# Performance work log

Measured on AMD Instinct MI355X. Metric: run time of the kernel, lower is better.

Reference implementation:

```python
import jax, jax.numpy as jnp
import numpy as np

NEG_SLOPE = 0.01  # torch F.leaky_relu default


def _mlp_block(x, mask, W, b):
    # x: [B,P,V,F]; mask: [B,P,V] bool; W: [H,F]; b: [H]
    h = jax.nn.leaky_relu(jnp.einsum('bpvf,hf->bpvh', x, W) + b, NEG_SLOPE)
    m = mask[..., None]
    out = jnp.where(m, h, 0.0)                                   # zeros at masked-out slots
    neg = jnp.where(m, out, -jnp.inf)
    pool = jnp.max(neg, axis=2, keepdims=True)                   # [B,P,1,H] masked max-pool
    any_valid = jnp.any(mask, axis=2)[:, :, None, None]
    pool = jnp.where(any_valid, pool, 0.0)                       # fully-masked polylines -> 0
    rep = jnp.broadcast_to(pool, out.shape)
    return jnp.concatenate([out, rep], axis=-1)                  # [B,P,V,2H]


def setup_inputs() -> dict:
    key = jax.random.key(0)
    ks = jax.random.split(key, 8)
    B, P, V, F, H = 32, 512, 32, 16, 64
    input_var = jax.random.normal(ks[0], (B, P, V, F), dtype=jnp.float32)
    input_mask = jax.random.bernoulli(ks[1], 0.8, (B, P, V))
    s = 1.0 / np.sqrt(F)
    W1 = jax.random.uniform(ks[2], (H, F), jnp.float32, -s, s)
    b1 = jax.random.uniform(ks[3], (H,), jnp.float32, -s, s)
    s2 = 1.0 / np.sqrt(2 * H)
    W2 = jax.random.uniform(ks[4], (H, 2 * H), jnp.float32, -s2, s2)
    b2 = jax.random.uniform(ks[5], (H,), jnp.float32, -s2, s2)
    W3 = jax.random.uniform(ks[6], (H, 2 * H), jnp.float32, -s2, s2)
    b3 = jax.random.uniform(ks[7], (H,), jnp.float32, -s2, s2)
    return {"input_var": input_var, "input_mask": input_mask,
            "W1": W1, "b1": b1, "W2": W2, "b2": b2, "W3": W3, "b3": b3,
            "size1": P, "size2": V}


def reference(input_var, input_mask, W1, b1, W2, b2, W3, b3, size1, size2):
    hidden = W1.shape[0]
    x = _mlp_block(input_var, input_mask, W1, b1)
    y = _mlp_block(x, input_mask, W2, b2)
    z = _mlp_block(y, input_mask, W3, b3)
    out = z[:, :, 0, -hidden:]                                   # pooled half, same across V
    out = jnp.where(jnp.any(input_mask, axis=2)[..., None], out, 0.0)
    return out
```

## Files before the change

kernel.cpp:

```cpp
#include <hip/hip_runtime.h>
#include <math.h>

namespace {
constexpr int kXS = 72;
constexpr float kSlope = 0.01f;

typedef short bf16x8 __attribute__((ext_vector_type(8)));
typedef float f32x4  __attribute__((ext_vector_type(4)));

__device__ __forceinline__ float lrelu(float x) { return fmaxf(x, kSlope * x); }

__device__ __forceinline__ unsigned short bfrne(float a) {
    union { float f; unsigned u; } v; v.f = a;
    return (unsigned short)((v.u + 0x7FFFu + ((v.u >> 16) & 1u)) >> 16);
}

__global__ void prep_weights(const float* __restrict__ W1,
                             const float* __restrict__ W2,
                             const float* __restrict__ W3,
                             unsigned short* __restrict__ ws)
{
    int t = blockIdx.x * blockDim.x + threadIdx.x;
    if (t >= 36 * 64) return;
    int f = t >> 6, l = t & 63, c = l & 15, q = l >> 4;
    unsigned short v[8] = {0, 0, 0, 0, 0, 0, 0, 0};
    const float* src = nullptr; int row = 0, k0 = 0, K = 0;
    if (f < 4) {
        if (q < 2) { src = W1; row = 16 * f + c; k0 = q * 8; K = 16; }
    } else if (f < 20) {
        int g = f - 4;  src = W2; row = 16 * (g >> 2) + c; k0 = (g & 3) * 32 + q * 8; K = 128;
    } else {
        int g = f - 20; src = W3; row = 16 * (g >> 2) + c; k0 = (g & 3) * 32 + q * 8; K = 128;
    }
    if (src) {
        #pragma unroll
        for (int j = 0; j < 8; ++j) v[j] = bfrne(src[row * K + k0 + j]);
    }
    unsigned short* dst = ws + (size_t)f * 512 + l * 8;
    *(ushort4*)(dst)     = make_ushort4(v[0], v[1], v[2], v[3]);
    *(ushort4*)(dst + 4) = make_ushort4(v[4], v[5], v[6], v[7]);
}

__global__ __launch_bounds__(256, 4) void fused_mlp_v5(
    const float* __restrict__ X, const int* __restrict__ M,
    const unsigned short* __restrict__ WF,
    const float* __restrict__ B1, const float* __restrict__ B2,
    const float* __restrict__ B3, float* __restrict__ OUT)
{
    __shared__ __align__(16) short sX[4][2][32 * kXS];
    __shared__ __align__(16) short sP[4][2][64];

    const int t = threadIdx.x, w = t >> 6, l = t & 63, c = l & 15, q = l >> 4;
    const size_t bp = (size_t)blockIdx.x * 4 + w;

    short* xb2 = &sX[w][0][0]; short* pl2 = &sP[w][0][0];
    short* xb3 = &sX[w][1][0]; short* pl3 = &sP[w][1][0];

    float4 xr[2][2];
    if (q < 2) {
        #pragma unroll
        for (int mt = 0; mt < 2; ++mt) {
            const float4* p = (const float4*)(X + (bp * 32 + 16 * mt + c) * 16 + q * 8);
            xr[mt][0] = p[0]; xr[mt][1] = p[1];
        }
    }
    const int4* Mp = (const int4*)(M + bp * 32);
    const int4 mr0 = Mp[q], mr1 = Mp[4 + q];
    const unsigned mbits =
        (mr0.x ? 1u : 0u)  | (mr0.y ? 2u : 0u)  | (mr0.z ? 4u : 0u)  | (mr0.w ? 8u : 0u) |
        (mr1.x ? 16u : 0u) | (mr1.y ? 32u : 0u) | (mr1.z ? 64u : 0u) | (mr1.w ? 128u : 0u);
    const bool anyv = __any(mbits != 0);

    float bias1[4], bias2[4], bias3[4];
    #pragma unroll
    for (int nt = 0; nt < 4; ++nt) {
        bias1[nt] = B1[16 * nt + c];
        bias2[nt] = B2[16 * nt + c];
        bias3[nt] = B3[16 * nt + c];
    }

    f32x4 acc[2][4];

    {
        bf16x8 a1f[2];
        #pragma unroll
        for (int mt = 0; mt < 2; ++mt) {
            bf16x8 v = {};
            if (q < 2) {
                float4 f0 = xr[mt][0], f1 = xr[mt][1];
                v[0] = (short)bfrne(f0.x); v[1] = (short)bfrne(f0.y);
                v[2] = (short)bfrne(f0.z); v[3] = (short)bfrne(f0.w);
                v[4] = (short)bfrne(f1.x); v[5] = (short)bfrne(f1.y);
                v[6] = (short)bfrne(f1.z); v[7] = (short)bfrne(f1.w);
            }
            a1f[mt] = v;
        }
        #pragma unroll
        for (int nt = 0; nt < 4; ++nt) {
            bf16x8 wf = *(const bf16x8*)(WF + (size_t)nt * 512 + l * 8);
            f32x4 c0 = { bias1[nt], bias1[nt], bias1[nt], bias1[nt] };
            acc[0][nt] = __builtin_amdgcn_mfma_f32_16x16x32_bf16(a1f[0], wf, c0, 0, 0, 0);
            acc[1][nt] = __builtin_amdgcn_mfma_f32_16x16x32_bf16(a1f[1], wf, c0, 0, 0, 0);
        }
    }

    auto epilogue = [&](short* xb, short* pl) {
        float pool[4];
        #pragma unroll
        for (int nt = 0; nt < 4; ++nt) {
            float pv = -INFINITY;
            #pragma unroll
            for (int mt = 0; mt < 2; ++mt) {
                short* base = &xb[(16 * mt + 4 * q) * kXS + 16 * nt + c];
                #pragma unroll
                for (int r = 0; r < 4; ++r) {
                    float y = lrelu(acc[mt][nt][r]);
                    bool mk = (mbits >> (mt * 4 + r)) & 1;
                    float o = mk ? y : 0.f;
                    pv = mk ? fmaxf(pv, y) : pv;
                    base[r * kXS] = (short)bfrne(o);
                }
            }
            pv = fmaxf(pv, __shfl_xor(pv, 16));
            pv = fmaxf(pv, __shfl_xor(pv, 32));
            pool[nt] = anyv ? pv : 0.f;
        }
        float ps = (q & 2) ? ((q & 1) ? pool[3] : pool[2])
                           : ((q & 1) ? pool[1] : pool[0]);
        pl[16 * q + c] = (short)bfrne(ps);
    };

    auto layerK = [&](const short* xb, const short* pl, int fb, const float (&bias)[4]) {
        bf16x8 a00 = *(const bf16x8*)&xb[(     c) * kXS      + q * 8];
        bf16x8 a01 = *(const bf16x8*)&xb[(16 + c) * kXS      + q * 8];
        bf16x8 a10 = *(const bf16x8*)&xb[(     c) * kXS + 32 + q * 8];
        bf16x8 a11 = *(const bf16x8*)&xb[(16 + c) * kXS + 32 + q * 8];
        bf16x8 ap0 = *(const bf16x8*)&pl[q * 8];
        bf16x8 ap1 = *(const bf16x8*)&pl[32 + q * 8];
        #pragma unroll
        for (int nt = 0; nt < 4; ++nt) {
            acc[0][nt] = f32x4{ bias[nt], bias[nt], bias[nt], bias[nt] };
            acc[1][nt] = acc[0][nt];
        }
        #pragma unroll
        for (int ks = 0; ks < 4; ++ks) {
            bf16x8 am0 = (ks == 0) ? a00 : (ks == 1) ? a10 : (ks == 2) ? ap0 : ap1;
            bf16x8 am1 = (ks == 0) ? a01 : (ks == 1) ? a11 : (ks == 2) ? ap0 : ap1;
            #pragma unroll
            for (int nt = 0; nt < 4; ++nt) {
                bf16x8 wf = *(const bf16x8*)(WF + ((size_t)(fb + nt * 4 + ks)) * 512 + l * 8);
                acc[0][nt] = __builtin_amdgcn_mfma_f32_16x16x32_bf16(am0, wf, acc[0][nt], 0, 0, 0);
                acc[1][nt] = __builtin_amdgcn_mfma_f32_16x16x32_bf16(am1, wf, acc[1][nt], 0, 0, 0);
            }
        }
    };

    epilogue(xb2, pl2);
    layerK(xb2, pl2, 4, bias2);
    epilogue(xb3, pl3);
    layerK(xb3, pl3, 20, bias3);

    {
        float pool[4];
        #pragma unroll
        for (int nt = 0; nt < 4; ++nt) {
            float pv = -INFINITY;
            #pragma unroll
            for (int mt = 0; mt < 2; ++mt)
                #pragma unroll
                for (int r = 0; r < 4; ++r) {
                    bool mk = (mbits >> (mt * 4 + r)) & 1;
                    float y = lrelu(acc[mt][nt][r]);
                    pv = mk ? fmaxf(pv, y) : pv;
                }
            pv = fmaxf(pv, __shfl_xor(pv, 16));
            pv = fmaxf(pv, __shfl_xor(pv, 32));
            pool[nt] = anyv ? pv : 0.f;
        }
        float ps = (q & 2) ? ((q & 1) ? pool[3] : pool[2])
                           : ((q & 1) ? pool[1] : pool[0]);
        OUT[bp * 64 + 16 * q + c] = ps;
    }
}
}

extern "C" void kernel_launch(void* const* d_in, const int* in_sizes, int n_in,
                              void* d_out, int out_size, void* d_ws, size_t ws_size,
                              hipStream_t stream) {
    (void)in_sizes; (void)n_in; (void)ws_size; (void)out_size;
    const float* X  = (const float*)d_in[0];
    const int*   M  = (const int*)d_in[1];
    const float* W1 = (const float*)d_in[2];
    const float* B1 = (const float*)d_in[3];
    const float* W2 = (const float*)d_in[4];
    const float* B2 = (const float*)d_in[5];
    const float* W3 = (const float*)d_in[6];
    const float* B3 = (const float*)d_in[7];
    float* OUT = (float*)d_out;
    unsigned short* WF = (unsigned short*)d_ws;

    prep_weights<<<(36 * 64 + 255) / 256, 256, 0, stream>>>(W1, W2, W3, WF);
    fused_mlp_v5<<<4096, 256, 0, stream>>>(X, M, WF, B1, B2, B3, OUT);
}
```

Before: 116.6 us.

## Single-buffer LDS, raise occupancy, hardware bf16 pack converts, additive masking

The per-wave LDS staging is cut from two buffers to one, halving shared memory per block, and launch bounds now allow 8 blocks per CU. Layer-2 and layer-3 activations reuse the same buffer. Bias loads for those layers are deferred to just before use, and A-fragment loads are issued per k-step, both aimed at lowering register pressure. The software bf16 rounding is replaced by the packed v_cvt_pk_bf16_f32 instruction, and masked max-pooling now adds a precomputed 0/-inf term instead of selecting. Masked slots are no longer zeroed before the next layer. This is safe because their rows only reach the output through the masked pool.

```diff
diff --git a/kernel.cpp b/kernel.cpp
--- a/kernel.cpp
+++ b/kernel.cpp
@@ -13,6 +13,12 @@
 __device__ __forceinline__ unsigned short bfrne(float a) {
     union { float f; unsigned u; } v; v.f = a;
     return (unsigned short)((v.u + 0x7FFFu + ((v.u >> 16) & 1u)) >> 16);
+}
+
+__device__ __forceinline__ unsigned cvtpk(float lo, float hi) {
+    unsigned r;
+    asm("v_cvt_pk_bf16_f32 %0, %1, %2" : "=v"(r) : "v"(lo), "v"(hi));
+    return r;
 }
 
 __global__ void prep_weights(const float* __restrict__ W1,
@@ -41,20 +47,20 @@
     *(ushort4*)(dst + 4) = make_ushort4(v[4], v[5], v[6], v[7]);
 }
 
-__global__ __launch_bounds__(256, 4) void fused_mlp_v5(
+__global__ __launch_bounds__(256, 8) void fused_mlp_v6(
     const float* __restrict__ X, const int* __restrict__ M,
     const unsigned short* __restrict__ WF,
     const float* __restrict__ B1, const float* __restrict__ B2,
     const float* __restrict__ B3, float* __restrict__ OUT)
 {
-    __shared__ __align__(16) short sX[4][2][32 * kXS];
-    __shared__ __align__(16) short sP[4][2][64];
+    __shared__ __align__(16) short sX[4][32 * kXS];
+    __shared__ __align__(16) short sP[4][64];
 
     const int t = threadIdx.x, w = t >> 6, l = t & 63, c = l & 15, q = l >> 4;
     const size_t bp = (size_t)blockIdx.x * 4 + w;
 
-    short* xb2 = &sX[w][0][0]; short* pl2 = &sP[w][0][0];
-    short* xb3 = &sX[w][1][0]; short* pl3 = &sP[w][1][0];
+    short* xb = &sX[w][0];
+    short* pl = &sP[w][0];
 
     float4 xr[2][2];
     if (q < 2) {
@@ -71,13 +77,14 @@
         (mr1.x ? 16u : 0u) | (mr1.y ? 32u : 0u) | (mr1.z ? 64u : 0u) | (mr1.w ? 128u : 0u);
     const bool anyv = __any(mbits != 0);
 
-    float bias1[4], bias2[4], bias3[4];
-    #pragma unroll
-    for (int nt = 0; nt < 4; ++nt) {
-        bias1[nt] = B1[16 * nt + c];
-        bias2[nt] = B2[16 * nt + c];
-        bias3[nt] = B3[16 * nt + c];
-    }
+    float addm[8];
+    #pragma unroll
+    for (int i = 0; i < 8; ++i)
+        addm[i] = ((mbits >> i) & 1u) ? 0.f : -INFINITY;
+
+    float bias1[4];
+    #pragma unroll
+    for (int nt = 0; nt < 4; ++nt) bias1[nt] = B1[16 * nt + c];
 
     f32x4 acc[2][4];
 
@@ -85,15 +92,14 @@
         bf16x8 a1f[2];
         #pragma unroll
         for (int mt = 0; mt < 2; ++mt) {
-            bf16x8 v = {};
+            union { bf16x8 v; unsigned u[4]; } cv; cv.v = bf16x8{};
             if (q < 2) {
-                float4 f0 = xr[mt][0], f1 = xr[mt][1];
-                v[0] = (short)bfrne(f0.x); v[1] = (short)bfrne(f0.y);
-                v[2] = (short)bfrne(f0.z); v[3] = (short)bfrne(f0.w);
-                v[4] = (short)bfrne(f1.x); v[5] = (short)bfrne(f1.y);
-                v[6] = (short)bfrne(f1.z); v[7] = (short)bfrne(f1.w);
-            }
-            a1f[mt] = v;
+                cv.u[0] = cvtpk(xr[mt][0].x, xr[mt][0].y);
+                cv.u[1] = cvtpk(xr[mt][0].z, xr[mt][0].w);
+                cv.u[2] = cvtpk(xr[mt][1].x, xr[mt][1].y);
+                cv.u[3] = cvtpk(xr[mt][1].z, xr[mt][1].w);
+            }
+            a1f[mt] = cv.v;
         }
         #pragma unroll
         for (int nt = 0; nt < 4; ++nt) {
@@ -104,22 +110,28 @@
         }
     }
 
-    auto epilogue = [&](short* xb, short* pl) {
+    auto epilogue = [&](short* xb_, short* pl_) {
         float pool[4];
         #pragma unroll
         for (int nt = 0; nt < 4; ++nt) {
             float pv = -INFINITY;
             #pragma unroll
             for (int mt = 0; mt < 2; ++mt) {
-                short* base = &xb[(16 * mt + 4 * q) * kXS + 16 * nt + c];
-                #pragma unroll
-                for (int r = 0; r < 4; ++r) {
-                    float y = lrelu(acc[mt][nt][r]);
-                    bool mk = (mbits >> (mt * 4 + r)) & 1;
-                    float o = mk ? y : 0.f;
-                    pv = mk ? fmaxf(pv, y) : pv;
-                    base[r * kXS] = (short)bfrne(o);
-                }
+                short* base = &xb_[(16 * mt + 4 * q) * kXS + 16 * nt + c];
+                float y0 = lrelu(acc[mt][nt][0]);
+                float y1 = lrelu(acc[mt][nt][1]);
+                float y2 = lrelu(acc[mt][nt][2]);
+                float y3 = lrelu(acc[mt][nt][3]);
+                pv = fmaxf(pv, y0 + addm[mt * 4 + 0]);
+                pv = fmaxf(pv, y1 + addm[mt * 4 + 1]);
+                pv = fmaxf(pv, y2 + addm[mt * 4 + 2]);
+                pv = fmaxf(pv, y3 + addm[mt * 4 + 3]);
+                unsigned u01 = cvtpk(y0, y1);
+                unsigned u23 = cvtpk(y2, y3);
+                base[0 * kXS] = (short)u01;
+                base[1 * kXS] = (short)(u01 >> 16);
+                base[2 * kXS] = (short)u23;
+                base[3 * kXS] = (short)(u23 >> 16);
             }
             pv = fmaxf(pv, __shfl_xor(pv, 16));
             pv = fmaxf(pv, __shfl_xor(pv, 32));
@@ -127,16 +139,11 @@
         }
         float ps = (q & 2) ? ((q & 1) ? pool[3] : pool[2])
                            : ((q & 1) ? pool[1] : pool[0]);
-        pl[16 * q + c] = (short)bfrne(ps);
+        pl_[16 * q + c] = (short)cvtpk(ps, ps);
     };
 
-    auto layerK = [&](const short* xb, const short* pl, int fb, const float (&bias)[4]) {
-        bf16x8 a00 = *(const bf16x8*)&xb[(     c) * kXS      + q * 8];
-        bf16x8 a01 = *(const bf16x8*)&xb[(16 + c) * kXS      + q * 8];
-        bf16x8 a10 = *(const bf16x8*)&xb[(     c) * kXS + 32 + q * 8];
-        bf16x8 a11 = *(const bf16x8*)&xb[(16 + c) * kXS + 32 + q * 8];
-        bf16x8 ap0 = *(const bf16x8*)&pl[q * 8];
-        bf16x8 ap1 = *(const bf16x8*)&pl[32 + q * 8];
+    auto layerK = [&](const short* xb_, const short* pl_, int fb,
+                      const float (&bias)[4]) {
         #pragma unroll
         for (int nt = 0; nt < 4; ++nt) {
             acc[0][nt] = f32x4{ bias[nt], bias[nt], bias[nt], bias[nt] };
@@ -144,8 +151,14 @@
         }
         #pragma unroll
         for (int ks = 0; ks < 4; ++ks) {
-            bf16x8 am0 = (ks == 0) ? a00 : (ks == 1) ? a10 : (ks == 2) ? ap0 : ap1;
-            bf16x8 am1 = (ks == 0) ? a01 : (ks == 1) ? a11 : (ks == 2) ? ap0 : ap1;
+            bf16x8 am0, am1;
+            if (ks < 2) {
+                am0 = *(const bf16x8*)&xb_[(     c) * kXS + ks * 32 + q * 8];
+                am1 = *(const bf16x8*)&xb_[(16 + c) * kXS + ks * 32 + q * 8];
+            } else {
+                am0 = *(const bf16x8*)&pl_[(ks - 2) * 32 + q * 8];
+                am1 = am0;
+            }
             #pragma unroll
             for (int nt = 0; nt < 4; ++nt) {
                 bf16x8 wf = *(const bf16x8*)(WF + ((size_t)(fb + nt * 4 + ks)) * 512 + l * 8);
@@ -155,10 +168,17 @@
         }
     };
 
-    epilogue(xb2, pl2);
-    layerK(xb2, pl2, 4, bias2);
-    epilogue(xb3, pl3);
-    layerK(xb3, pl3, 20, bias3);
+    epilogue(xb, pl);
+    float bias2[4];
+    #pragma unroll
+    for (int nt = 0; nt < 4; ++nt) bias2[nt] = B2[16 * nt + c];
+    layerK(xb, pl, 4, bias2);
+
+    epilogue(xb, pl);
+    float bias3[4];
+    #pragma unroll
+    for (int nt = 0; nt < 4; ++nt) bias3[nt] = B3[16 * nt + c];
+    layerK(xb, pl, 20, bias3);
 
     {
         float pool[4];
@@ -168,11 +188,8 @@
             #pragma unroll
             for (int mt = 0; mt < 2; ++mt)
                 #pragma unroll
-                for (int r = 0; r < 4; ++r) {
-                    bool mk = (mbits >> (mt * 4 + r)) & 1;
-                    float y = lrelu(acc[mt][nt][r]);
-                    pv = mk ? fmaxf(pv, y) : pv;
-                }
+                for (int r = 0; r < 4; ++r)
+                    pv = fmaxf(pv, lrelu(acc[mt][nt][r]) + addm[mt * 4 + r]);
             pv = fmaxf(pv, __shfl_xor(pv, 16));
             pv = fmaxf(pv, __shfl_xor(pv, 32));
             pool[nt] = anyv ? pv : 0.f;
@@ -200,5 +217,5 @@
     unsigned short* WF = (unsigned short*)d_ws;
 
     prep_weights<<<(36 * 64 + 255) / 256, 256, 0, stream>>>(W1, W2, W3, WF);
-    fused_mlp_v5<<<4096, 256, 0, stream>>>(X, M, WF, B1, B2, B3, OUT);
-}
+    fused_mlp_v6<<<4096, 256, 0, stream>>>(X, M, WF, B1, B2, B3, OUT);
+}
```

Result: slower. 127.4 us (+9.3%).
